# Kernel optimization log

Measured on AMD Instinct MI355X. Metric: run time of the kernel, lower is better.

## Reference

```python
import jax, jax.numpy as jnp
import numpy as np

EPS = 1e-6

def setup_inputs() -> dict:
    key = jax.random.key(0)
    k1, k2, k3 = jax.random.split(key, 3)
    B, N, F, OUT = 16, 1024, 64, 128
    x = jax.random.normal(k1, (B, N, F), dtype=jnp.float32)
    A = jax.random.uniform(k2, (B, N, N), dtype=jnp.float32)
    kernel = jax.random.normal(k3, (3 * F, OUT), dtype=jnp.float32) * 0.05
    bias = jnp.zeros((OUT,), dtype=jnp.float32)
    return {"x": x, "A": A, "kernel": kernel, "bias": bias}


def reference(x, A, kernel, bias):
    # x: [B,N,F], A: [B,N,N]
    n = A.shape[-1]
    eye = jnp.eye(n, dtype=A.dtype)
    Az = A * (1.0 - eye)          # zero out diagonal (A -= diag(diag_part(A)))
    A_hat = Az + eye              # add self-loops
    deg = A_hat.sum(axis=2)       # [B,N]
    inv_asym = 1.0 / (EPS + deg)                 # D^{-1}
    s = 1.0 / (EPS + jnp.sqrt(deg))              # D^{-1/2}
    # Three message-passing variants; apply diagonal scalings as broadcasts
    o1 = jnp.matmul(Az, x)                                   # A x
    o2 = inv_asym[:, :, None] * jnp.matmul(A_hat, x)         # D^{-1} A_hat x
    o3 = s[:, :, None] * jnp.matmul(A_hat, s[:, :, None] * x)  # D^{-1/2} A_hat D^{-1/2} x
    out = jnp.concatenate([o1, o2, o3], axis=-1)             # [B,N,3F]
    out = jnp.matmul(out, kernel) + bias                     # [B,N,OUT]
    return jax.nn.relu(out)
```

## Files before the change

### kernel.cpp

```cpp
#include <hip/hip_runtime.h>
#include <hip/hip_bf16.h>
#include <cstdint>

#define NN    1024
#define FF    64
#define OUTF  128
#define KCAT  192
#define EPSV  1e-6f

typedef __attribute__((ext_vector_type(4))) float  f32x4;
typedef __attribute__((ext_vector_type(8))) __bf16 bf16x8;
typedef __attribute__((ext_vector_type(4))) __bf16 bf16x4;

#define MFMA16(a, b, c) __builtin_amdgcn_mfma_f32_16x16x32_bf16(a, b, c, 0, 0, 0)
#define GLOAD_LDS16(g, l)                                          \
    __builtin_amdgcn_global_load_lds(                              \
        (const __attribute__((address_space(1))) void*)(g),        \
        (__attribute__((address_space(3))) void*)(l), 16, 0, 0)

__global__ __launch_bounds__(256) void k_deg_cvt(const float* __restrict__ A,
                                                 float* __restrict__ d1,
                                                 float* __restrict__ sArr,
                                                 __bf16* __restrict__ Az) {
    int wave = threadIdx.x >> 6;
    int lane = threadIdx.x & 63;
    int row  = blockIdx.x * 4 + wave;
    int i    = row & (NN - 1);
    const f32x4* rp = (const f32x4*)(A + (size_t)row * NN);
    __bf16* op = Az + (size_t)row * NN;
    float sum = 0.f;
#pragma unroll
    for (int t = 0; t < 4; ++t) {
        f32x4 v = rp[t * 64 + lane];
        int base = (t * 64 + lane) * 4;
#pragma unroll
        for (int q = 0; q < 4; ++q)
            if (base + q == i) v[q] = 0.f;
        sum += v[0] + v[1] + v[2] + v[3];
        bf16x4 o;
#pragma unroll
        for (int q = 0; q < 4; ++q) o[q] = (__bf16)v[q];
        *(bf16x4*)(op + base) = o;
    }
#pragma unroll
    for (int off = 32; off; off >>= 1) sum += __shfl_xor(sum, off);
    if (lane == 0) {
        float deg = 1.0f + sum;
        d1[row]   = 1.0f / (EPSV + deg);
        sArr[row] = 1.0f / (EPSV + sqrtf(deg));
    }
}

__global__ __launch_bounds__(256) void k_prep(const float* __restrict__ x,
                                              const float* __restrict__ sArr,
                                              const float* __restrict__ kern,
                                              __bf16* __restrict__ xT,
                                              __bf16* __restrict__ sxT,
                                              __bf16* __restrict__ KT) {
    __shared__ float tile[64][65];
    int bid = blockIdx.x;
    int b   = bid >> 4;
    int k0  = (bid & 15) * 64;
    const float* xp = x + ((size_t)b * NN + k0) * FF;
    for (int i = threadIdx.x; i < 64 * 64; i += 256) {
        int r = i >> 6, c = i & 63;
        tile[r][c] = xp[r * FF + c];
    }
    __syncthreads();
    for (int i = threadIdx.x; i < 64 * 64; i += 256) {
        int c = i >> 6, kk = i & 63;
        float v  = tile[kk][c];
        float sv = v * sArr[b * NN + k0 + kk];
        size_t o = ((size_t)b * FF + c) * NN + k0 + kk;
        xT[o]  = (__bf16)v;
        sxT[o] = (__bf16)sv;
    }
    if (threadIdx.x < 96) {
        int idx = bid * 96 + threadIdx.x;
        int c = idx / KCAT;
        int k = idx - c * KCAT;
        KT[idx] = (__bf16)kern[k * OUTF + c];
    }
}

__global__ __launch_bounds__(512, 4) void k_main(const __bf16* __restrict__ Az,
                                                 const float* __restrict__ x,
                                                 const float* __restrict__ bias,
                                                 const float* __restrict__ d1g,
                                                 const float* __restrict__ sg,
                                                 const __bf16* __restrict__ xT,
                                                 const __bf16* __restrict__ sxT,
                                                 const __bf16* __restrict__ KT,
                                                 float* __restrict__ out) {
    __shared__ __align__(16) char smem[81920];

    const int tid  = threadIdx.x;
    const int w    = tid >> 6;
    const int lane = tid & 63;
    const int l15  = lane & 15;
    const int hi   = lane >> 4;
    const int h8   = hi * 8;

    const int idx  = (blockIdx.x & 7) * 64 + (blockIdx.x >> 3);
    const int b    = idx >> 5;
    const int row0 = (idx & 31) * 32;

    const int rA = 4 * w + hi;
    const int sA = (l15 ^ (rA & 7)) * 8;
    const __bf16* Asrc = Az + (size_t)(b * NN + row0 + rA) * NN + sA;

    const int f0 = 4 * w + hi;
    const int s0 = (l15 ^ (f0 & 7)) * 8;
    const int f1 = 32 + 4 * w + hi;
    const int s1 = (l15 ^ (f1 & 7)) * 8;
    const __bf16* Xsrc0 = xT  + (size_t)(b * FF + f0) * NN + s0;
    const __bf16* Xsrc1 = xT  + (size_t)(b * FF + f1) * NN + s1;
    const __bf16* Ssrc0 = sxT + (size_t)(b * FF + f0) * NN + s0;
    const __bf16* Ssrc1 = sxT + (size_t)(b * FF + f1) * NN + s1;

#define STAGE(t, pb)                                                     \
    {                                                                    \
        char* bb = smem + (pb) * 40960;                                  \
        const int ko = (t) * 128;                                        \
        GLOAD_LDS16(Asrc + ko,  bb + w * 1024);                          \
        GLOAD_LDS16(Xsrc0 + ko, bb + 8192  + w * 1024);                  \
        GLOAD_LDS16(Xsrc1 + ko, bb + 8192  + (w + 8) * 1024);            \
        GLOAD_LDS16(Ssrc0 + ko, bb + 24576 + w * 1024);                  \
        GLOAD_LDS16(Ssrc1 + ko, bb + 24576 + (w + 8) * 1024);            \
    }

    STAGE(0, 0)
    STAGE(1, 1)

    const int rg = w >> 2;
    const int fg = w & 3;

    const int arow = rg * 16 + l15;
    const int frow = fg * 16 + l15;
    const int swz  = (l15 & 7) << 4;
    const int aBase = arow * 256;
    const int xBase = 8192 + frow * 256;
    const int sBase = 24576 + frow * 256;

    f32x4 P = {}, Q = {};
#pragma unroll
    for (int t = 0; t < 8; ++t) {
        if (t < 7) { asm volatile("s_waitcnt vmcnt(5)" ::: "memory"); }
        else       { asm volatile("s_waitcnt vmcnt(0)" ::: "memory"); }
        __builtin_amdgcn_s_barrier();
        __builtin_amdgcn_sched_barrier(0);
        {
            const char* bb = smem + (t & 1) * 40960;
#pragma unroll
            for (int ks = 0; ks < 4; ++ks) {
                const int ko = (ks * 64 + hi * 16) ^ swz;
                bf16x8 a  = *(const bf16x8*)(bb + aBase + ko);
                bf16x8 xf = *(const bf16x8*)(bb + xBase + ko);
                bf16x8 sf = *(const bf16x8*)(bb + sBase + ko);
                P = MFMA16(a, xf, P);
                Q = MFMA16(a, sf, Q);
            }
        }
        asm volatile("s_waitcnt lgkmcnt(0)" ::: "memory");
        __builtin_amdgcn_sched_barrier(0);
        __builtin_amdgcn_s_barrier();
        if (t < 6) STAGE(t + 2, t & 1)
    }
#undef STAGE

    __bf16 (*os)[216] = (__bf16(*)[216])smem;
#pragma unroll
    for (int j = 0; j < 4; ++j) {
        int rr   = rg * 16 + hi * 4 + j;
        int grow = b * NN + row0 + rr;
        float dv = d1g[grow];
        float sv = sg[grow];
        int cc   = fg * 16 + l15;
        float xv = x[(size_t)grow * FF + cc];
        os[rr][cc]       = (__bf16)P[j];
        os[rr][64 + cc]  = (__bf16)(dv * (P[j] + xv));
        os[rr][128 + cc] = (__bf16)(sv * (Q[j] + sv * xv));
    }
    __syncthreads();

    const int rge = w >> 2;
    const int cge = w & 3;
    f32x4 e0 = {}, e1 = {};
#pragma unroll
    for (int ks = 0; ks < 6; ++ks) {
        bf16x8 of = *(const bf16x8*)&os[rge * 16 + l15][ks * 32 + h8];
        bf16x8 k0 = *(const bf16x8*)&KT[(size_t)(cge * 32 + l15) * KCAT + ks * 32 + h8];
        bf16x8 k1 = *(const bf16x8*)&KT[(size_t)(cge * 32 + 16 + l15) * KCAT + ks * 32 + h8];
        e0 = MFMA16(k0, of, e0);
        e1 = MFMA16(k1, of, e1);
    }
    {
        const size_t orow = (size_t)(b * NN + row0 + rge * 16 + l15) * OUTF;
#pragma unroll
        for (int g = 0; g < 2; ++g) {
            f32x4 ev = g ? e1 : e0;
            int col0 = cge * 32 + g * 16 + hi * 4;
            f32x4 bv = *(const f32x4*)&bias[col0];
            f32x4 rv;
#pragma unroll
            for (int j = 0; j < 4; ++j) {
                float v = ev[j] + bv[j];
                rv[j] = v > 0.f ? v : 0.f;
            }
            *(f32x4*)&out[orow + col0] = rv;
        }
    }
}

extern "C" void kernel_launch(void* const* d_in, const int* in_sizes, int n_in,
                              void* d_out, int out_size, void* d_ws, size_t ws_size,
                              hipStream_t stream) {
    const float* x    = (const float*)d_in[0];
    const float* A    = (const float*)d_in[1];
    const float* kern = (const float*)d_in[2];
    const float* bias = (const float*)d_in[3];
    float* out = (float*)d_out;

    char* ws = (char*)d_ws;
    __bf16* Az  = (__bf16*)(ws);
    float*  d1  = (float*)(ws + 33554432);
    float*  s   = (float*)(ws + 33554432 + 65536);
    __bf16* xT  = (__bf16*)(ws + 33554432 + 131072);
    __bf16* sxT = (__bf16*)(ws + 33554432 + 131072 + 2097152);
    __bf16* KT  = (__bf16*)(ws + 33554432 + 131072 + 2 * 2097152);
    (void)ws_size; (void)in_sizes; (void)n_in; (void)out_size;

    k_deg_cvt<<<dim3(4096), dim3(256), 0, stream>>>(A, d1, s, Az);
    k_prep<<<dim3(256), dim3(256), 0, stream>>>(x, s, kern, xT, sxT, KT);
    k_main<<<dim3(512), dim3(512), 0, stream>>>(Az, x, bias, d1, s, xT, sxT, KT, out);
}
```

Measured before the change: 127.0 us.

## Compute s-scaled x on the fly and triple-buffer main-loop staging

Drops the precomputed sxT array. The main kernel now loads the per-node s vector into LDS once and forms s*x in registers from the staged x tile before each MFMA. The double-buffered loop with a trailing barrier becomes a three-buffer ring that issues the next stage right after the leading barrier, removing one barrier and the lgkmcnt wait per iteration. This cuts global and LDS traffic for the x operand and the prep kernel's writes, at the cost of extra per-element convert and multiply work in the MFMA loop.

```diff
diff --git a/kernel.cpp b/kernel.cpp
--- a/kernel.cpp
+++ b/kernel.cpp
@@ -52,10 +52,8 @@
 }
 
 __global__ __launch_bounds__(256) void k_prep(const float* __restrict__ x,
-                                              const float* __restrict__ sArr,
                                               const float* __restrict__ kern,
                                               __bf16* __restrict__ xT,
-                                              __bf16* __restrict__ sxT,
                                               __bf16* __restrict__ KT) {
     __shared__ float tile[64][65];
     int bid = blockIdx.x;
@@ -69,11 +67,8 @@
     __syncthreads();
     for (int i = threadIdx.x; i < 64 * 64; i += 256) {
         int c = i >> 6, kk = i & 63;
-        float v  = tile[kk][c];
-        float sv = v * sArr[b * NN + k0 + kk];
         size_t o = ((size_t)b * FF + c) * NN + k0 + kk;
-        xT[o]  = (__bf16)v;
-        sxT[o] = (__bf16)sv;
+        xT[o] = (__bf16)tile[kk][c];
     }
     if (threadIdx.x < 96) {
         int idx = bid * 96 + threadIdx.x;
@@ -89,10 +84,9 @@
                                                  const float* __restrict__ d1g,
                                                  const float* __restrict__ sg,
                                                  const __bf16* __restrict__ xT,
-                                                 const __bf16* __restrict__ sxT,
                                                  const __bf16* __restrict__ KT,
                                                  float* __restrict__ out) {
-    __shared__ __align__(16) char smem[81920];
+    __shared__ __align__(16) char smem[77824];
 
     const int tid  = threadIdx.x;
     const int w    = tid >> 6;
@@ -113,58 +107,63 @@
     const int s0 = (l15 ^ (f0 & 7)) * 8;
     const int f1 = 32 + 4 * w + hi;
     const int s1 = (l15 ^ (f1 & 7)) * 8;
-    const __bf16* Xsrc0 = xT  + (size_t)(b * FF + f0) * NN + s0;
-    const __bf16* Xsrc1 = xT  + (size_t)(b * FF + f1) * NN + s1;
-    const __bf16* Ssrc0 = sxT + (size_t)(b * FF + f0) * NN + s0;
-    const __bf16* Ssrc1 = sxT + (size_t)(b * FF + f1) * NN + s1;
+    const __bf16* Xsrc0 = xT + (size_t)(b * FF + f0) * NN + s0;
+    const __bf16* Xsrc1 = xT + (size_t)(b * FF + f1) * NN + s1;
 
 #define STAGE(t, pb)                                                     \
     {                                                                    \
-        char* bb = smem + (pb) * 40960;                                  \
+        char* bb = smem + (pb) * 24576;                                  \
         const int ko = (t) * 128;                                        \
         GLOAD_LDS16(Asrc + ko,  bb + w * 1024);                          \
-        GLOAD_LDS16(Xsrc0 + ko, bb + 8192  + w * 1024);                  \
-        GLOAD_LDS16(Xsrc1 + ko, bb + 8192  + (w + 8) * 1024);            \
-        GLOAD_LDS16(Ssrc0 + ko, bb + 24576 + w * 1024);                  \
-        GLOAD_LDS16(Ssrc1 + ko, bb + 24576 + (w + 8) * 1024);            \
-    }
-
+        GLOAD_LDS16(Xsrc0 + ko, bb + 8192 + w * 1024);                   \
+        GLOAD_LDS16(Xsrc1 + ko, bb + 8192 + (w + 8) * 1024);             \
+    }
+
+    if (w < 4) {
+        GLOAD_LDS16(sg + (size_t)b * NN + w * 256 + lane * 4,
+                    smem + 73728 + w * 1024);
+    }
     STAGE(0, 0)
     STAGE(1, 1)
 
     const int rg = w >> 2;
     const int fg = w & 3;
 
-    const int arow = rg * 16 + l15;
-    const int frow = fg * 16 + l15;
-    const int swz  = (l15 & 7) << 4;
-    const int aBase = arow * 256;
-    const int xBase = 8192 + frow * 256;
-    const int sBase = 24576 + frow * 256;
+    const int swz   = (l15 & 7) << 4;
+    const int aBase = (rg * 16 + l15) * 256;
+    const int xBase = 8192 + (fg * 16 + l15) * 256;
+    const char* sVec = smem + 73728;
 
     f32x4 P = {}, Q = {};
 #pragma unroll
     for (int t = 0; t < 8; ++t) {
-        if (t < 7) { asm volatile("s_waitcnt vmcnt(5)" ::: "memory"); }
+        if (t < 7) { asm volatile("s_waitcnt vmcnt(3)" ::: "memory"); }
         else       { asm volatile("s_waitcnt vmcnt(0)" ::: "memory"); }
         __builtin_amdgcn_s_barrier();
         __builtin_amdgcn_sched_barrier(0);
+        if (t < 6) STAGE(t + 2, (t + 2) % 3)
+        __builtin_amdgcn_sched_barrier(0);
         {
-            const char* bb = smem + (t & 1) * 40960;
+            const char* bb = smem + (t % 3) * 24576;
+            const char* sT = sVec + t * 512;
 #pragma unroll
             for (int ks = 0; ks < 4; ++ks) {
                 const int ko = (ks * 64 + hi * 16) ^ swz;
                 bf16x8 a  = *(const bf16x8*)(bb + aBase + ko);
                 bf16x8 xf = *(const bf16x8*)(bb + xBase + ko);
-                bf16x8 sf = *(const bf16x8*)(bb + sBase + ko);
+                f32x4 sl = *(const f32x4*)(sT + ks * 128 + hi * 32);
+                f32x4 sh = *(const f32x4*)(sT + ks * 128 + hi * 32 + 16);
+                bf16x8 sf;
+#pragma unroll
+                for (int m = 0; m < 4; ++m) {
+                    sf[m]     = (__bf16)(sl[m] * (float)xf[m]);
+                    sf[m + 4] = (__bf16)(sh[m] * (float)xf[m + 4]);
+                }
                 P = MFMA16(a, xf, P);
                 Q = MFMA16(a, sf, Q);
             }
         }
-        asm volatile("s_waitcnt lgkmcnt(0)" ::: "memory");
         __builtin_amdgcn_sched_barrier(0);
-        __builtin_amdgcn_s_barrier();
-        if (t < 6) STAGE(t + 2, t & 1)
     }
 #undef STAGE
 
@@ -226,11 +225,10 @@
     float*  d1  = (float*)(ws + 33554432);
     float*  s   = (float*)(ws + 33554432 + 65536);
     __bf16* xT  = (__bf16*)(ws + 33554432 + 131072);
-    __bf16* sxT = (__bf16*)(ws + 33554432 + 131072 + 2097152);
-    __bf16* KT  = (__bf16*)(ws + 33554432 + 131072 + 2 * 2097152);
+    __bf16* KT  = (__bf16*)(ws + 33554432 + 131072 + 2097152);
     (void)ws_size; (void)in_sizes; (void)n_in; (void)out_size;
 
     k_deg_cvt<<<dim3(4096), dim3(256), 0, stream>>>(A, d1, s, Az);
-    k_prep<<<dim3(256), dim3(256), 0, stream>>>(x, s, kern, xT, sxT, KT);
-    k_main<<<dim3(512), dim3(512), 0, stream>>>(Az, x, bias, d1, s, xT, sxT, KT, out);
-}
+    k_prep<<<dim3(256), dim3(256), 0, stream>>>(x, kern, xT, KT);
+    k_main<<<dim3(512), dim3(512), 0, stream>>>(Az, x, bias, d1, s, xT, KT, out);
+}
```

Measured after the change: 128.1 us. About the same (+0.8%).
